# Kernel optimization log

Measured on AMD Instinct MI355X. Metric: run time of the kernel, lower is better.

The kernel has to match this reference:

```python
import jax, jax.numpy as jnp
import numpy as np

WH, WW = 7, 7
N = WH * WW
H = 16          # num_heads
D = 32          # head_dim
NW = 64         # num windows per image (mask.shape[0])


def _relative_position_index(wh, ww):
    coords = np.stack(np.meshgrid(np.arange(wh), np.arange(ww), indexing='ij'))  # (2, wh, ww)
    cf = coords.reshape(2, -1)                                                   # (2, N)
    rel = cf[:, :, None] - cf[:, None, :]                                        # (2, N, N)
    rel = rel.transpose(1, 2, 0).copy()
    rel[:, :, 0] += wh - 1
    rel[:, :, 1] += ww - 1
    rel[:, :, 0] *= 2 * ww - 1
    return rel.sum(-1)  # (N, N) int

REL_IDX = jnp.asarray(_relative_position_index(WH, WW))


def setup_inputs() -> dict:
    key = jax.random.key(0)
    ks = jax.random.split(key, 5)
    B_ = 2048
    dim = H * D
    x = jax.random.normal(ks[0], (B_, N, dim), dtype=jnp.float32)
    mask = jnp.zeros((NW, N, N), dtype=jnp.float32)
    rpb_table = jax.random.normal(ks[1], ((2 * WH - 1) * (2 * WW - 1), H), dtype=jnp.float32) * 0.02
    qkv_w = jax.random.normal(ks[2], (3 * dim, dim), dtype=jnp.float32) * (dim ** -0.5)
    qkv_b = jnp.zeros((3 * dim,), dtype=jnp.float32)
    proj_w = jax.random.normal(ks[3], (dim, dim), dtype=jnp.float32) * (dim ** -0.5)
    proj_b = jnp.zeros((dim,), dtype=jnp.float32)
    return {"x": x, "mask": mask, "rpb_table": rpb_table,
            "qkv_w": qkv_w, "qkv_b": qkv_b, "proj_w": proj_w, "proj_b": proj_b}


def reference(x, mask, rpb_table, qkv_w, qkv_b, proj_w, proj_b):
    B_, n, C = x.shape
    scale = D ** -0.5
    # qkv projection (torch Linear: x @ W^T + b)
    qkv = (x @ qkv_w.T + qkv_b).reshape(B_, n, 3, H, D)
    q = qkv[:, :, 0].transpose(0, 2, 1, 3) * scale  # (B_, H, N, D)
    k = qkv[:, :, 1].transpose(0, 2, 1, 3)
    v = qkv[:, :, 2].transpose(0, 2, 1, 3)
    attn = jnp.einsum('bhnd,bhmd->bhnm', q, k)      # (B_, H, N, N)
    # relative position bias: gather (N*N,) rows from table -> (N, N, H) -> (H, N, N)
    bias = rpb_table[REL_IDX.reshape(-1)].reshape(n, n, H).transpose(2, 0, 1)
    attn = attn + bias[None]
    # shifted-window mask add: (B, nW, H, N, N) + (1, nW, 1, N, N)
    nW = mask.shape[0]
    attn = attn.reshape(B_ // nW, nW, H, n, n) + mask[None, :, None]
    attn = attn.reshape(B_, H, n, n)
    attn = jax.nn.softmax(attn, axis=-1)
    out = jnp.einsum('bhnm,bhmd->bhnd', attn, v)    # (B_, H, N, D)
    out = out.transpose(0, 2, 1, 3).reshape(B_, n, H * D)
    return out @ proj_w.T + proj_b
```

## Files before the change

### kernel.cpp

```cpp
#include <hip/hip_runtime.h>

typedef _Float16 f16;
typedef _Float16 f16x8 __attribute__((ext_vector_type(8)));
typedef _Float16 f16x4 __attribute__((ext_vector_type(4)));
typedef float f32x4 __attribute__((ext_vector_type(4)));

#define NTOK 49
#define NH 16
#define HD 32
#define DIM 512
#define NWIN 64
#define NB 2048
#define MTOT (NB*NTOK)
#define SCALE 0.17677669529663687f
#define VTS 56

__device__ __forceinline__ void gload_lds16(const f16* g, f16* l) {
    __builtin_amdgcn_global_load_lds((const __attribute__((address_space(1))) void*)g,
                                     (__attribute__((address_space(3))) void*)l, 16, 0, 0);
}

__global__ __launch_bounds__(256) void cvt_f32_f16(const float* __restrict__ s,
                                                   f16* __restrict__ d, int n4) {
    int i = blockIdx.x * 256 + threadIdx.x;
    int st = gridDim.x * 256;
    for (; i < n4; i += st) {
        float4 v = ((const float4*)s)[i];
        f16x4 o = { (f16)v.x, (f16)v.y, (f16)v.z, (f16)v.w };
        *(f16x4*)(d + (size_t)i * 4) = o;
    }
}

__global__ __launch_bounds__(256) void build_comb2(const float* __restrict__ rpb,
                                                   const float* __restrict__ mask,
                                                   f16* __restrict__ comb2) {
    int idx = blockIdx.x * 256 + threadIdx.x;
    int r4   = idx & 3;
    int tj   = (idx >> 2) & 3;
    int ti   = (idx >> 4) & 3;
    int lane = (idx >> 6) & 63;
    int wh   = idx >> 12;
    int h = wh & 15, w = wh >> 4;
    int g = lane >> 4, c16 = lane & 15;
    int row = ti * 16 + g * 4 + r4;
    int col = tj * 16 + c16;
    float v = 0.f;
    if (row < NTOK && col < NTOK) {
        int ri = row / 7, ci = row - ri * 7;
        int rj = col / 7, cj = col - rj * 7;
        int rel = (ri - rj + 6) * 13 + (ci - cj + 6);
        v = rpb[rel * NH + h] + mask[(w * NTOK + row) * NTOK + col];
    }
    comb2[idx] = (f16)v;
}

#define WAIT_LGKM  asm volatile("s_waitcnt lgkmcnt(0)" ::: "memory")
#define WAIT_VM(N) asm volatile("s_waitcnt vmcnt(" #N ")" ::: "memory")

template<int MODE, int NT>
__global__ __launch_bounds__(512) void gemm_kernel(const f16* __restrict__ A,
                                                   const f16* __restrict__ Bw,
                                                   const float* __restrict__ bias,
                                                   f16* __restrict__ qo,
                                                   f16* __restrict__ ko,
                                                   f16* __restrict__ vto,
                                                   float* __restrict__ outp) {
    __shared__ __align__(16) f16 As[2][256][64];
    __shared__ __align__(16) f16 Bs[2][256][64];

    const int tid = threadIdx.x;
    const int lane = tid & 63;
    const int wv = tid >> 6;
    const int wm = wv >> 2, wn = wv & 3;
    const int g = lane >> 4, c16 = lane & 15;

    const int nblk = gridDim.x;
    const int f = blockIdx.x;
    const int work = (f & 7) * (nblk >> 3) + (f >> 3);
    const int m0 = (work / NT) * 256;
    const int n0 = (work % NT) * 256;

    const int srow = lane >> 3;
    const int schunk = (lane & 7) ^ srow;
    const f16* gA = A  + (size_t)(m0 + wv * 16 + srow) * DIM + schunk * 8;
    const f16* gB = Bw + (size_t)(n0 + wv * 16 + srow) * DIM + schunk * 8;

#define STAGE1(buf, kt, role) do {                                             \
    const f16* _s = (((role) < 2) ? gA : gB) + (size_t)(((role) & 1) * 128) * DIM + (kt) * 64; \
    f16* _d = ((role) < 2) ? &As[buf][((role) & 1) * 128 + wv * 16][0]         \
                           : &Bs[buf][((role) & 1) * 128 + wv * 16][0];        \
    gload_lds16(_s, _d);                                                       \
    gload_lds16(_s + (size_t)8 * DIM, _d + 8 * 64);                            \
} while (0)
#define STAGE_T(buf, kt) do { STAGE1(buf, kt, 0); STAGE1(buf, kt, 1);          \
                              STAGE1(buf, kt, 2); STAGE1(buf, kt, 3); } while (0)

#define READS(buf, kk, AF, BF) do {                                            \
    _Pragma("unroll") for (int _i = 0; _i < 8; ++_i)                           \
        (AF)[_i] = *(const f16x8*)&As[buf][wm * 128 + _i * 16 + c16][(((kk) * 4 + g) ^ (c16 & 7)) * 8]; \
    _Pragma("unroll") for (int _j = 0; _j < 4; ++_j)                           \
        (BF)[_j] = *(const f16x8*)&Bs[buf][wn * 64 + _j * 16 + c16][(((kk) * 4 + g) ^ (c16 & 7)) * 8]; \
} while (0)

#define MM(AF, BF) do {                                                        \
    __builtin_amdgcn_s_setprio(1);                                             \
    _Pragma("unroll") for (int _j = 0; _j < 4; ++_j)                           \
    _Pragma("unroll") for (int _i = 0; _i < 8; ++_i)                           \
        acc[_j][_i] = __builtin_amdgcn_mfma_f32_16x16x32_f16((BF)[_j], (AF)[_i], acc[_j][_i], 0, 0, 0); \
    __builtin_amdgcn_s_setprio(0);                                             \
} while (0)

    f32x4 acc[4][8];
#pragma unroll
    for (int j = 0; j < 4; ++j)
#pragma unroll
        for (int i = 0; i < 8; ++i)
            acc[j][i] = (f32x4){0.f, 0.f, 0.f, 0.f};

    f16x8 a0[8], b0[4], a1[8], b1[4];

    const int KT = DIM / 64;

    STAGE_T(0, 0);
    STAGE_T(1, 1);
    WAIT_VM(8);
    __builtin_amdgcn_s_barrier();
    READS(0, 0, a0, b0);

#pragma unroll
    for (int t = 0; t < KT; ++t) {
        const int b = t & 1, nb = b ^ 1;

        READS(b, 1, a1, b1);
        MM(a0, b0);
        WAIT_LGKM;
        __builtin_amdgcn_s_barrier();
        if (t + 2 < KT) STAGE_T(b, t + 2);
        if (t + 2 < KT) { WAIT_VM(8); }
        else if (t + 1 < KT) { WAIT_VM(0); }

        if (t + 1 < KT) READS(nb, 0, a0, b0);
        MM(a1, b1);
    }
#undef STAGE1
#undef STAGE_T
#undef READS
#undef MM

#pragma unroll
    for (int i = 0; i < 8; ++i) {
        const int m = m0 + wm * 128 + i * 16 + c16;
        int bb = 0, tk = 0;
        if (MODE == 0) { bb = m / NTOK; tk = m - bb * NTOK; }
#pragma unroll
        for (int j = 0; j < 4; ++j) {
            const int n = n0 + wn * 64 + j * 16 + g * 4;
            f32x4 v = acc[j][i];
            const f32x4 b4 = *(const f32x4*)&bias[n];
            v += b4;
            if (MODE == 0) {
                const int s = n >> 9;
                const int hh = (n >> 5) & 15;
                const int d0 = n & 31;
                const size_t bh = (size_t)(bb * NH + hh);
                if (s == 0) {
                    f16x4 o = { (f16)(v[0] * SCALE), (f16)(v[1] * SCALE),
                                (f16)(v[2] * SCALE), (f16)(v[3] * SCALE) };
                    *(f16x4*)(qo + (bh * NTOK + tk) * HD + d0) = o;
                } else if (s == 1) {
                    f16x4 o = { (f16)v[0], (f16)v[1], (f16)v[2], (f16)v[3] };
                    *(f16x4*)(ko + (bh * NTOK + tk) * HD + d0) = o;
                } else {
#pragma unroll
                    for (int r = 0; r < 4; ++r)
                        vto[(bh * HD + d0 + r) * VTS + tk] = (f16)v[r];
                }
            } else {
                float4 o = { v[0], v[1], v[2], v[3] };
                *(float4*)(outp + (size_t)m * DIM + n) = o;
            }
        }
    }
}

__global__ __launch_bounds__(256) void attn_kernel(const f16* __restrict__ qw,
                                                   const f16* __restrict__ kw,
                                                   const f16* __restrict__ vt,
                                                   const f16* __restrict__ comb2,
                                                   f16* __restrict__ aout) {
    __shared__ __align__(16) f16 Ps[4][64][72];

    const int wv = threadIdx.x >> 6;
    const int l = threadIdx.x & 63;
    const int f = blockIdx.x;
    const int work = (f & 7) * (gridDim.x >> 3) + (f >> 3);
    const int bid = work * 4 + wv;
    const int b = bid >> 4, h = bid & 15;
    const int w = b & (NWIN - 1);
    const int g = l >> 4, c16 = l & 15;
    const size_t qkbase = (size_t)bid * (NTOK * HD);
    const size_t vbase = (size_t)bid * (HD * VTS);

    const f16x8 z8 = {};

    f16x8 qf[4], kf[4];
#pragma unroll
    for (int t = 0; t < 4; ++t) {
        int row = t * 16 + c16;
        f16x8 q = z8, k = z8;
        if (row < NTOK) {
            q = *(const f16x8*)(qw + qkbase + row * HD + g * 8);
            k = *(const f16x8*)(kw + qkbase + row * HD + g * 8);
        }
        qf[t] = q; kf[t] = k;
    }

    const f16* cb = comb2 + (((size_t)(w * NH + h) * 64 + l) << 6);
    f16x8 cbv[8];
#pragma unroll
    for (int k = 0; k < 8; ++k) cbv[k] = *(const f16x8*)(cb + k * 8);
    f32x4 S[4][4];
#pragma unroll
    for (int i = 0; i < 4; ++i)
#pragma unroll
        for (int j = 0; j < 4; ++j) {
            const int e = i * 16 + j * 4;
#pragma unroll
            for (int r = 0; r < 4; ++r)
                S[i][j][r] = (float)cbv[(e + r) >> 3][(e + r) & 7];
        }
#pragma unroll
    for (int i = 0; i < 4; ++i)
#pragma unroll
        for (int j = 0; j < 4; ++j)
            S[i][j] = __builtin_amdgcn_mfma_f32_16x16x32_f16(qf[i], kf[j], S[i][j], 0, 0, 0);

#pragma unroll
    for (int ti = 0; ti < 4; ++ti)
#pragma unroll
        for (int r = 0; r < 4; ++r) {
            int row = ti * 16 + g * 4 + r;
            float v0 = S[ti][0][r], v1 = S[ti][1][r], v2 = S[ti][2][r];
            float v3 = (c16 == 0) ? S[ti][3][r] : -1e30f;
            float mx = fmaxf(fmaxf(v0, v1), fmaxf(v2, v3));
#pragma unroll
            for (int mk = 1; mk < 16; mk <<= 1) mx = fmaxf(mx, __shfl_xor(mx, mk, 64));
            float p0 = __expf(v0 - mx), p1 = __expf(v1 - mx), p2 = __expf(v2 - mx);
            float p3 = (c16 == 0) ? __expf(v3 - mx) : 0.f;
            float sm = p0 + p1 + p2 + p3;
#pragma unroll
            for (int mk = 1; mk < 16; mk <<= 1) sm += __shfl_xor(sm, mk, 64);
            float inv = 1.f / sm;
            Ps[wv][row][c16]      = (f16)(p0 * inv);
            Ps[wv][row][16 + c16] = (f16)(p1 * inv);
            Ps[wv][row][32 + c16] = (f16)(p2 * inv);
            Ps[wv][row][48 + c16] = (f16)(p3 * inv);
        }
    __syncthreads();

    f32x4 O2[2][4];
    const f32x4 zf = (f32x4){0.f, 0.f, 0.f, 0.f};
#pragma unroll
    for (int td = 0; td < 2; ++td)
#pragma unroll
        for (int ti = 0; ti < 4; ++ti) O2[td][ti] = zf;
#pragma unroll
    for (int c = 0; c < 2; ++c) {
        f16x8 pf[4], vf[2];
#pragma unroll
        for (int ti = 0; ti < 4; ++ti)
            pf[ti] = *(const f16x8*)&Ps[wv][ti * 16 + c16][c * 32 + g * 8];
        int tcol = c * 32 + g * 8;
#pragma unroll
        for (int td = 0; td < 2; ++td) {
            f16x8 vv = z8;
            if (tcol < VTS)
                vv = *(const f16x8*)(vt + vbase + (size_t)(td * 16 + c16) * VTS + tcol);
            vf[td] = vv;
        }
#pragma unroll
        for (int td = 0; td < 2; ++td)
#pragma unroll
            for (int ti = 0; ti < 4; ++ti)
                O2[td][ti] = __builtin_amdgcn_mfma_f32_16x16x32_f16(vf[td], pf[ti], O2[td][ti], 0, 0, 0);
    }

#pragma unroll
    for (int ti = 0; ti < 4; ++ti) {
        int tok = ti * 16 + c16;
        if (tok < NTOK) {
            size_t ob = ((size_t)(b * NTOK + tok)) * DIM + h * HD;
#pragma unroll
            for (int td = 0; td < 2; ++td) {
                f32x4 v = O2[td][ti];
                f16x4 o = { (f16)v[0], (f16)v[1], (f16)v[2], (f16)v[3] };
                *(f16x4*)(aout + ob + td * 16 + g * 4) = o;
            }
        }
    }
}

extern "C" void kernel_launch(void* const* d_in, const int* in_sizes, int n_in,
                              void* d_out, int out_size, void* d_ws, size_t ws_size,
                              hipStream_t stream) {
    const float* x      = (const float*)d_in[0];
    const float* mask   = (const float*)d_in[1];
    const float* rpb    = (const float*)d_in[2];
    const float* qkv_w  = (const float*)d_in[3];
    const float* qkv_b  = (const float*)d_in[4];
    const float* proj_w = (const float*)d_in[5];
    const float* proj_b = (const float*)d_in[6];
    float* out = (float*)d_out;

    char* ws = (char*)d_ws;
    size_t o = 0;
    f16* x16   = (f16*)(ws + o); o += (size_t)MTOT * DIM * 2;
    f16* w16   = (f16*)(ws + o); o += (size_t)1536 * 512 * 2;
    f16* pw16  = (f16*)(ws + o); o += (size_t)512 * 512 * 2;
    f16* qws   = (f16*)(ws + o); o += (size_t)NB * NH * NTOK * HD * 2;
    f16* kws   = (f16*)(ws + o); o += (size_t)NB * NH * NTOK * HD * 2;
    f16* vtws  = (f16*)(ws + o); o += (size_t)NB * NH * HD * VTS * 2;
    f16* cb2   = (f16*)(ws + o);
    f16* aout = x16;

    cvt_f32_f16<<<dim3(2048), dim3(256), 0, stream>>>(x, x16, MTOT * DIM / 4);
    cvt_f32_f16<<<dim3(768), dim3(256), 0, stream>>>(qkv_w, w16, 1536 * 512 / 4);
    cvt_f32_f16<<<dim3(256), dim3(256), 0, stream>>>(proj_w, pw16, 512 * 512 / 4);

    build_comb2<<<dim3(16384), dim3(256), 0, stream>>>(rpb, mask, cb2);

    gemm_kernel<0, 6><<<dim3((MTOT / 256) * 6), dim3(512), 0, stream>>>(
        x16, w16, qkv_b, qws, kws, vtws, nullptr);

    attn_kernel<<<dim3(NB * NH / 4), dim3(256), 0, stream>>>(qws, kws, vtws, cb2, aout);

    gemm_kernel<1, 2><<<dim3((MTOT / 256) * 2), dim3(512), 0, stream>>>(
        aout, pw16, proj_b, nullptr, nullptr, nullptr, out);
}
```

Before: 571.2 us.

## Transpose attention scores, defer softmax normalization, and fuse prep kernels

```diff
diff --git a/kernel.cpp b/kernel.cpp
--- a/kernel.cpp
+++ b/kernel.cpp
@@ -3,6 +3,7 @@
 typedef _Float16 f16;
 typedef _Float16 f16x8 __attribute__((ext_vector_type(8)));
 typedef _Float16 f16x4 __attribute__((ext_vector_type(4)));
+typedef __fp16 fp16x2 __attribute__((ext_vector_type(2)));
 typedef float f32x4 __attribute__((ext_vector_type(4)));
 
 #define NTOK 49
@@ -20,10 +21,10 @@
                                      (__attribute__((address_space(3))) void*)l, 16, 0, 0);
 }
 
-__global__ __launch_bounds__(256) void cvt_f32_f16(const float* __restrict__ s,
-                                                   f16* __restrict__ d, int n4) {
-    int i = blockIdx.x * 256 + threadIdx.x;
-    int st = gridDim.x * 256;
+__device__ __forceinline__ void cvt_body(const float* __restrict__ s, f16* __restrict__ d,
+                                         int n4, int bid, int nb) {
+    int i = bid * 256 + threadIdx.x;
+    int st = nb * 256;
     for (; i < n4; i += st) {
         float4 v = ((const float4*)s)[i];
         f16x4 o = { (f16)v.x, (f16)v.y, (f16)v.z, (f16)v.w };
@@ -31,10 +32,25 @@
     }
 }
 
-__global__ __launch_bounds__(256) void build_comb2(const float* __restrict__ rpb,
+__global__ __launch_bounds__(256) void cvt_f32_f16(const float* __restrict__ s,
+                                                   f16* __restrict__ d, int n4) {
+    cvt_body(s, d, n4, blockIdx.x, gridDim.x);
+}
+
+__global__ __launch_bounds__(256) void prep_kernel(const float* __restrict__ rpb,
                                                    const float* __restrict__ mask,
-                                                   f16* __restrict__ comb2) {
-    int idx = blockIdx.x * 256 + threadIdx.x;
+                                                   f16* __restrict__ comb2,
+                                                   const float* __restrict__ qkvw,
+                                                   f16* __restrict__ w16,
+                                                   const float* __restrict__ projw,
+                                                   f16* __restrict__ pw16) {
+    const int bid = blockIdx.x;
+    if (bid >= 16384) {
+        if (bid < 16384 + 768) cvt_body(qkvw, w16, 1536 * 512 / 4, bid - 16384, 768);
+        else                   cvt_body(projw, pw16, 512 * 512 / 4, bid - 16384 - 768, 256);
+        return;
+    }
+    int idx = bid * 256 + threadIdx.x;
     int r4   = idx & 3;
     int tj   = (idx >> 2) & 3;
     int ti   = (idx >> 4) & 3;
@@ -42,14 +58,16 @@
     int wh   = idx >> 12;
     int h = wh & 15, w = wh >> 4;
     int g = lane >> 4, c16 = lane & 15;
-    int row = ti * 16 + g * 4 + r4;
-    int col = tj * 16 + c16;
-    float v = 0.f;
-    if (row < NTOK && col < NTOK) {
-        int ri = row / 7, ci = row - ri * 7;
-        int rj = col / 7, cj = col - rj * 7;
-        int rel = (ri - rj + 6) * 13 + (ci - cj + 6);
-        v = rpb[rel * NH + h] + mask[(w * NTOK + row) * NTOK + col];
+    int k = ti * 16 + g * 4 + r4;
+    int q = tj * 16 + c16;
+    float v;
+    if (k >= NTOK)      v = -30000.f;
+    else if (q >= NTOK) v = 0.f;
+    else {
+        int rq = q / 7, cq = q - rq * 7;
+        int rk = k / 7, ck = k - rk * 7;
+        int rel = (rq - rk + 6) * 13 + (cq - ck + 6);
+        v = rpb[rel * NH + h] + mask[(w * NTOK + q) * NTOK + k];
     }
     comb2[idx] = (f16)v;
 }
@@ -219,7 +237,7 @@
     f16x8 cbv[8];
 #pragma unroll
     for (int k = 0; k < 8; ++k) cbv[k] = *(const f16x8*)(cb + k * 8);
-    f32x4 S[4][4];
+    f32x4 St[4][4];
 #pragma unroll
     for (int i = 0; i < 4; ++i)
 #pragma unroll
@@ -227,36 +245,50 @@
             const int e = i * 16 + j * 4;
 #pragma unroll
             for (int r = 0; r < 4; ++r)
-                S[i][j][r] = (float)cbv[(e + r) >> 3][(e + r) & 7];
+                St[i][j][r] = (float)cbv[(e + r) >> 3][(e + r) & 7];
         }
 #pragma unroll
     for (int i = 0; i < 4; ++i)
 #pragma unroll
         for (int j = 0; j < 4; ++j)
-            S[i][j] = __builtin_amdgcn_mfma_f32_16x16x32_f16(qf[i], kf[j], S[i][j], 0, 0, 0);
-
-#pragma unroll
-    for (int ti = 0; ti < 4; ++ti)
-#pragma unroll
-        for (int r = 0; r < 4; ++r) {
-            int row = ti * 16 + g * 4 + r;
-            float v0 = S[ti][0][r], v1 = S[ti][1][r], v2 = S[ti][2][r];
-            float v3 = (c16 == 0) ? S[ti][3][r] : -1e30f;
-            float mx = fmaxf(fmaxf(v0, v1), fmaxf(v2, v3));
-#pragma unroll
-            for (int mk = 1; mk < 16; mk <<= 1) mx = fmaxf(mx, __shfl_xor(mx, mk, 64));
-            float p0 = __expf(v0 - mx), p1 = __expf(v1 - mx), p2 = __expf(v2 - mx);
-            float p3 = (c16 == 0) ? __expf(v3 - mx) : 0.f;
-            float sm = p0 + p1 + p2 + p3;
-#pragma unroll
-            for (int mk = 1; mk < 16; mk <<= 1) sm += __shfl_xor(sm, mk, 64);
-            float inv = 1.f / sm;
-            Ps[wv][row][c16]      = (f16)(p0 * inv);
-            Ps[wv][row][16 + c16] = (f16)(p1 * inv);
-            Ps[wv][row][32 + c16] = (f16)(p2 * inv);
-            Ps[wv][row][48 + c16] = (f16)(p3 * inv);
-        }
-    __syncthreads();
+            St[i][j] = __builtin_amdgcn_mfma_f32_16x16x32_f16(kf[i], qf[j], St[i][j], 0, 0, 0);
+
+    float inv[4];
+#pragma unroll
+    for (int j = 0; j < 4; ++j) {
+        float m = St[0][j][0];
+#pragma unroll
+        for (int i = 0; i < 4; ++i)
+#pragma unroll
+            for (int r = 0; r < 4; ++r) m = fmaxf(m, St[i][j][r]);
+        m = fmaxf(m, __shfl_xor(m, 16, 64));
+        m = fmaxf(m, __shfl_xor(m, 32, 64));
+        float s = 0.f;
+#pragma unroll
+        for (int i = 0; i < 4; ++i)
+#pragma unroll
+            for (int r = 0; r < 4; ++r) {
+                float p = __expf(St[i][j][r] - m);
+                St[i][j][r] = p;
+                s += p;
+            }
+        s += __shfl_xor(s, 16, 64);
+        s += __shfl_xor(s, 32, 64);
+        inv[j] = 1.f / s;
+    }
+
+#pragma unroll
+    for (int j = 0; j < 4; ++j) {
+        const int q = j * 16 + c16;
+#pragma unroll
+        for (int i = 0; i < 4; ++i) {
+            fp16x2 u0 = __builtin_amdgcn_cvt_pkrtz(St[i][j][0], St[i][j][1]);
+            fp16x2 u1 = __builtin_amdgcn_cvt_pkrtz(St[i][j][2], St[i][j][3]);
+            *(fp16x2*)&Ps[wv][q][i * 16 + 4 * g]     = u0;
+            *(fp16x2*)&Ps[wv][q][i * 16 + 4 * g + 2] = u1;
+        }
+    }
+    WAIT_LGKM;
 
     f32x4 O2[2][4];
     const f32x4 zf = (f32x4){0.f, 0.f, 0.f, 0.f};
@@ -293,7 +325,9 @@
 #pragma unroll
             for (int td = 0; td < 2; ++td) {
                 f32x4 v = O2[td][ti];
-                f16x4 o = { (f16)v[0], (f16)v[1], (f16)v[2], (f16)v[3] };
+                float iv = inv[ti];
+                f16x4 o = { (f16)(v[0] * iv), (f16)(v[1] * iv),
+                            (f16)(v[2] * iv), (f16)(v[3] * iv) };
                 *(f16x4*)(aout + ob + td * 16 + g * 4) = o;
             }
         }
@@ -324,10 +358,9 @@
     f16* aout = x16;
 
     cvt_f32_f16<<<dim3(2048), dim3(256), 0, stream>>>(x, x16, MTOT * DIM / 4);
-    cvt_f32_f16<<<dim3(768), dim3(256), 0, stream>>>(qkv_w, w16, 1536 * 512 / 4);
-    cvt_f32_f16<<<dim3(256), dim3(256), 0, stream>>>(proj_w, pw16, 512 * 512 / 4);
-
-    build_comb2<<<dim3(16384), dim3(256), 0, stream>>>(rpb, mask, cb2);
+
+    prep_kernel<<<dim3(16384 + 768 + 256), dim3(256), 0, stream>>>(
+        rpb, mask, cb2, qkv_w, w16, proj_w, pw16);
 
     gemm_kernel<0, 6><<<dim3((MTOT / 256) * 6), dim3(512), 0, stream>>>(
         x16, w16, qkv_b, qws, kws, vtws, nullptr);
```

After: 542.6 us. -5.0%, faster.
